# Kernel optimization log

Measured on AMD Instinct MI355X. Metric: run time of the kernel, lower is better.

## Reference

```python
import jax, jax.numpy as jnp
import numpy as np

B, T, E, H, P = 512, 512, 64, 128, 96


def setup_inputs() -> dict:
    key = jax.random.key(0)
    ks = jax.random.split(key, 12)
    s = 1.0 / np.sqrt(H)  # torch GRU/Linear uniform init scale
    u = lambda k, shape: jax.random.uniform(k, shape, jnp.float32, -s, s)
    return {
        "x": jax.random.normal(ks[0], (B, T, E), jnp.float32),
        "W_ih0": u(ks[1], (3 * H, E)),
        "W_hh0": u(ks[2], (3 * H, H)),
        "b_ih0": u(ks[3], (3 * H,)),
        "b_hh0": u(ks[4], (3 * H,)),
        "W_ih1": u(ks[5], (3 * H, H)),
        "W_hh1": u(ks[6], (3 * H, H)),
        "b_ih1": u(ks[7], (3 * H,)),
        "b_hh1": u(ks[8], (3 * H,)),
        "W_head": u(ks[9], (P, H)),
        "b_head": u(ks[10], (P,)),
    }


def _gru_layer(x, W_ih, W_hh, b_ih, b_hh):
    # x: [B, T, F]; PyTorch gate order: r, z, n
    Bn, Tn, _ = x.shape
    Hn = W_hh.shape[1]
    # precompute input-side gates for all timesteps: [B, T, 3H]
    xg = jnp.einsum('btf,gf->btg', x, W_ih) + b_ih

    def step(h, xg_t):
        hg = h @ W_hh.T + b_hh                      # [B, 3H]
        xr, xz, xn = jnp.split(xg_t, 3, axis=-1)
        hr, hz, hn = jnp.split(hg, 3, axis=-1)
        r = jax.nn.sigmoid(xr + hr)
        z = jax.nn.sigmoid(xz + hz)
        n = jnp.tanh(xn + r * hn)
        h_new = (1.0 - z) * n + z * h
        return h_new, h_new

    h0 = jnp.zeros((Bn, Hn), x.dtype)
    _, ys = jax.lax.scan(step, h0, jnp.swapaxes(xg, 0, 1))  # ys: [T, B, H]
    return jnp.swapaxes(ys, 0, 1)                            # [B, T, H]


def reference(x, W_ih0, W_hh0, b_ih0, b_hh0, W_ih1, W_hh1, b_ih1, b_hh1, W_head, b_head):
    h1 = _gru_layer(x, W_ih0, W_hh0, b_ih0, b_hh0)
    h2 = _gru_layer(h1, W_ih1, W_hh1, b_ih1, b_hh1)
    last = h2[:, -1, :]                   # [B, H]
    return last @ W_head.T + b_head       # [B, pred_len]
```

## Files before the change

### kernel.cpp

```cpp
#include <hip/hip_runtime.h>


#define B_SZ 512
#define T_SZ 512
#define E_SZ 64
#define H_SZ 128
#define P_SZ 96
#define NB   16
#define NGRP (B_SZ / NB)
#define LO_SCALE 2048.0f
#define LO_INV   (1.0f/2048.0f)
#define SC_SIG  (-1.44269504f)
#define SC_TANH (-2.88539008f)

typedef _Float16 half8 __attribute__((ext_vector_type(8)));
typedef float    f32x4 __attribute__((ext_vector_type(4)));

__device__ __forceinline__ float exp2_(float x) {
#if __has_builtin(__builtin_amdgcn_exp2f)
    return __builtin_amdgcn_exp2f(x);
#else
    return exp2f(x);
#endif
}
__device__ __forceinline__ float rcp_(float x) {
#if __has_builtin(__builtin_amdgcn_rcpf)
    return __builtin_amdgcn_rcpf(x);
#else
    return 1.0f / x;
#endif
}

__device__ __forceinline__ int swz256(int row, int byte) {
    return row * 256 + (byte ^ ((row & 7) << 4));
}

__device__ __forceinline__ void load_bfrag(const float* __restrict__ W, int ldk,
                                           int n0, int kt, int ln, float scale,
                                           half8* hi, half8* lo) {
    int n = n0 + (ln & 15);
    int k = kt * 32 + (ln >> 4) * 8;
    const float* p = W + (size_t)n * ldk + k;
    float4 a = *(const float4*)p;
    float4 b = *(const float4*)(p + 4);
    float v[8] = {a.x, a.y, a.z, a.w, b.x, b.y, b.z, b.w};
    half8 h, l;
    #pragma unroll
    for (int j = 0; j < 8; ++j) {
        float w = v[j] * scale;
        _Float16 hh = (_Float16)w;
        h[j] = hh;
        l[j] = (_Float16)((w - (float)hh) * LO_SCALE);
    }
    *hi = h;
    if (lo) *lo = l;
}

#define LOADX(Sx, tt)                                                              \
    if ((tt) < T_SZ) {                                                             \
        _Pragma("unroll") for (int kt = 0; kt < KFX; ++kt)                         \
            Sx[kt] = *(const half8*)(xlane + (size_t)(tt) * ROWB + kt * 64);       \
    }

#define GRU_STEP(Sx, tcur, tnext)                                                  \
    {                                                                              \
        const char* hb = hs[(tcur) & 1];                                           \
        half8 ah[4];                                                               \
        _Pragma("unroll") for (int kt = 0; kt < 4; ++kt)                           \
            ah[kt] = *(const half8*)(hb + swz256(colg, kt * 64 + rgrp * 16));      \
        f32x4 ax0 = {bs0, bs0, bs0, bs0};                                          \
        f32x4 ax1 = {bs1, bs1, bs1, bs1};                                          \
        f32x4 ax2 = {bi2s, bi2s, bi2s, bi2s};                                      \
        f32x4 ah2 = {bh2s, bh2s, bh2s, bh2s};                                      \
        f32x4 ah0 = {0.f, 0.f, 0.f, 0.f};                                          \
        f32x4 ah1 = ah0, al2 = ah0;                                                \
        _Pragma("unroll") for (int kt = 0; kt < KFX; ++kt) {                       \
            ax0 = __builtin_amdgcn_mfma_f32_16x16x32_f16(Sx[kt], bx[0][kt], ax0, 0, 0, 0); \
            ax1 = __builtin_amdgcn_mfma_f32_16x16x32_f16(Sx[kt], bx[1][kt], ax1, 0, 0, 0); \
            ax2 = __builtin_amdgcn_mfma_f32_16x16x32_f16(Sx[kt], bx[2][kt], ax2, 0, 0, 0); \
        }                                                                          \
        _Pragma("unroll") for (int kt = 0; kt < 4; ++kt) {                         \
            ah0 = __builtin_amdgcn_mfma_f32_16x16x32_f16(ah[kt], bhh[0][kt], ah0, 0, 0, 0); \
            ah1 = __builtin_amdgcn_mfma_f32_16x16x32_f16(ah[kt], bhh[1][kt], ah1, 0, 0, 0); \
            ah2 = __builtin_amdgcn_mfma_f32_16x16x32_f16(ah[kt], bhh[2][kt], ah2, 0, 0, 0); \
            al2 = __builtin_amdgcn_mfma_f32_16x16x32_f16(ah[kt], bhl2[kt],   al2, 0, 0, 0); \
        }                                                                          \
        LOADX(Sx, tnext)                                                           \
        float hn_[4];                                                              \
        _Pragma("unroll") for (int j = 0; j < 4; ++j) {                            \
            float e0 = exp2_(ax0[j] + ah0[j]);                                     \
            float rr = rcp_(1.f + e0);                                             \
            float e1 = exp2_(ax1[j] + ah1[j]);                                     \
            float zz = rcp_(1.f + e1);                                             \
            float hnv = ah2[j] + al2[j] * LO_INV;                                  \
            float v  = ax2[j] + rr * hnv;                                          \
            v = fminf(fmaxf(v, -60.f), 60.f);                                      \
            float e2 = exp2_(v);                                                   \
            float nn = (1.f - e2) * rcp_(1.f + e2);                                \
            hn_[j] = nn + zz * (hreg[j] - nn);                                     \
            hreg[j] = hn_[j];                                                      \
        }                                                                          \
        char* hw = hs[((tcur) + 1) & 1];                                           \
        _Pragma("unroll") for (int j = 0; j < 4; ++j) {                            \
            int bb = rgrp * 4 + j;                                                 \
            *(_Float16*)(hw + swz256(bb, cw * 2)) = (_Float16)hn_[j];              \
            if constexpr (OUT_ALL) {                                               \
                ((_Float16*)hout)[((size_t)(b0 + bb) * T_SZ + (tcur)) * H_SZ + cw] \
                    = (_Float16)hn_[j];                                            \
            } else {                                                               \
                if ((tcur) == T_SZ - 1)                                            \
                    ((float*)hout)[(size_t)(b0 + bb) * H_SZ + cw] = hn_[j];        \
            }                                                                      \
        }                                                                          \
           \
        asm volatile("s_waitcnt lgkmcnt(0)" ::: "memory");                         \
        __builtin_amdgcn_s_barrier();                                              \
        __builtin_amdgcn_sched_barrier(0);                                         \
    }

template<int K_IN, bool OUT_ALL, int ROLE>
__device__ __forceinline__ void gru_body(const _Float16* __restrict__ xin,
                                         const float* __restrict__ W_ih,
                                         const float* __restrict__ W_hh,
                                         const float* __restrict__ b_ih,
                                         const float* __restrict__ b_hh,
                                         void* __restrict__ hout,
                                         int* __restrict__ prog,
                                         int grp, char (*hs)[4096])
{
    constexpr int KFX  = K_IN / 32;
    constexpr int ROWB = K_IN * 2;

    const int tid  = threadIdx.x;
    const int ln   = tid & 63;
    const int wv   = tid >> 6;
    const int colg = ln & 15;
    const int rgrp = ln >> 4;
    const int b0   = grp * NB;
    const int cw   = wv * 16 + colg;

    half8 bx[3][KFX];
    half8 bhh[3][4];
    half8 bhl2[4];
    const float gsc[3] = {SC_SIG, SC_SIG, SC_TANH};
    #pragma unroll
    for (int g = 0; g < 3; ++g) {
        int n0 = g * 128 + wv * 16;
        #pragma unroll
        for (int kt = 0; kt < KFX; ++kt)
            load_bfrag(W_ih, K_IN, n0, kt, ln, gsc[g], &bx[g][kt], nullptr);
        #pragma unroll
        for (int kt = 0; kt < 4; ++kt)
            load_bfrag(W_hh, H_SZ, n0, kt, ln, gsc[g], &bhh[g][kt],
                       (g == 2) ? &bhl2[kt] : nullptr);
    }
    const float bs0  = SC_SIG  * (b_ih[cw] + b_hh[cw]);
    const float bs1  = SC_SIG  * (b_ih[128 + cw] + b_hh[128 + cw]);
    const float bi2s = SC_TANH * b_ih[256 + cw];
    const float bh2s = SC_TANH * b_hh[256 + cw];

    if (tid < 256) *(float4*)(hs[0] + tid * 16) = make_float4(0.f, 0.f, 0.f, 0.f);
    float hreg[4] = {0.f, 0.f, 0.f, 0.f};

    const char* xlane = (const char*)xin
        + (size_t)(b0 + colg) * T_SZ * ROWB
        + rgrp * 16;

    int avail = 0;
    if (ROLE == 1) {
        while (avail < 4) {
            avail = __hip_atomic_load(prog, __ATOMIC_ACQUIRE, __HIP_MEMORY_SCOPE_AGENT);
            if (avail < 4) __builtin_amdgcn_s_sleep(8);
        }
    }

    half8 Ax[KFX], Bx2[KFX];
    LOADX(Ax, 0)
    LOADX(Bx2, 1)
    __syncthreads();

    for (int t = 0; t < T_SZ; t += 2) {
        if (ROLE == 1 && avail < T_SZ) {
            const int need = (t + 4 < T_SZ) ? t + 4 : T_SZ;
            while (avail < need) {
                avail = __hip_atomic_load(prog, __ATOMIC_ACQUIRE, __HIP_MEMORY_SCOPE_AGENT);
                if (avail < need) __builtin_amdgcn_s_sleep(8);
            }
        }
        GRU_STEP(Ax,  t,     t + 2)
        GRU_STEP(Bx2, t + 1, t + 3)
        if (ROLE == 0 && (t & 7) == 6) {
            asm volatile("s_waitcnt vmcnt(0)" ::: "memory");
            __builtin_amdgcn_s_barrier();
            if (tid == 0)
                __hip_atomic_store(prog, t + 2, __ATOMIC_RELEASE, __HIP_MEMORY_SCOPE_AGENT);
        }
    }
}

__global__ __launch_bounds__(512)
void gru_fused(const _Float16* __restrict__ xh,
               _Float16* __restrict__ h1,
               float* __restrict__ h2,
               const float* __restrict__ W_ih0, const float* __restrict__ W_hh0,
               const float* __restrict__ b_ih0, const float* __restrict__ b_hh0,
               const float* __restrict__ W_ih1, const float* __restrict__ W_hh1,
               const float* __restrict__ b_ih1, const float* __restrict__ b_hh1,
               int* __restrict__ prog)
{
    __shared__ __align__(16) char hs[2][4096];
    const int role = blockIdx.x >> 5;
    const int grp  = blockIdx.x & 31;
    if (role == 0)
        gru_body<E_SZ, true, 0>(xh, W_ih0, W_hh0, b_ih0, b_hh0, h1, prog + grp, grp, hs);
    else
        gru_body<H_SZ, false, 1>(h1, W_ih1, W_hh1, b_ih1, b_hh1, h2, prog + grp, grp, hs);
}

__global__ __launch_bounds__(256)
void cvt_f32_f16(const float* __restrict__ in, _Float16* __restrict__ out, int n8)
{
    int i = blockIdx.x * 256 + threadIdx.x;
    if (i >= n8) return;
    const float4* p = (const float4*)in + (size_t)i * 2;
    float4 a = p[0];
    float4 b = p[1];
    half8 h;
    h[0] = (_Float16)a.x; h[1] = (_Float16)a.y; h[2] = (_Float16)a.z; h[3] = (_Float16)a.w;
    h[4] = (_Float16)b.x; h[5] = (_Float16)b.y; h[6] = (_Float16)b.z; h[7] = (_Float16)b.w;
    ((half8*)out)[i] = h;
}

__global__ __launch_bounds__(256)
void head_kernel(const float* __restrict__ h2,
                 const float* __restrict__ W,
                 const float* __restrict__ bias,
                 float* __restrict__ out)
{
    int idx = blockIdx.x * 256 + threadIdx.x;
    if (idx >= B_SZ * P_SZ) return;
    int b = idx / P_SZ;
    int p = idx % P_SZ;
    const float* hv = h2 + b * H_SZ;
    const float* wv = W + p * H_SZ;
    float a0 = 0.f, a1 = 0.f, a2 = 0.f, a3 = 0.f;
    #pragma unroll
    for (int i = 0; i < H_SZ; i += 4) {
        float4 h4 = *(const float4*)(hv + i);
        float4 w4 = *(const float4*)(wv + i);
        a0 += h4.x * w4.x;
        a1 += h4.y * w4.y;
        a2 += h4.z * w4.z;
        a3 += h4.w * w4.w;
    }
    out[idx] = (a0 + a1) + (a2 + a3) + bias[p];
}

extern "C" void kernel_launch(void* const* d_in, const int* in_sizes, int n_in,
                              void* d_out, int out_size, void* d_ws, size_t ws_size,
                              hipStream_t stream)
{
    const float* x      = (const float*)d_in[0];
    const float* W_ih0  = (const float*)d_in[1];
    const float* W_hh0  = (const float*)d_in[2];
    const float* b_ih0  = (const float*)d_in[3];
    const float* b_hh0  = (const float*)d_in[4];
    const float* W_ih1  = (const float*)d_in[5];
    const float* W_hh1  = (const float*)d_in[6];
    const float* b_ih1  = (const float*)d_in[7];
    const float* b_hh1  = (const float*)d_in[8];
    const float* W_head = (const float*)d_in[9];
    const float* b_head = (const float*)d_in[10];
    float* out = (float*)d_out;

    char* ws = (char*)d_ws;
    _Float16* h1  = (_Float16*)ws;
    _Float16* xh  = (_Float16*)(ws + (64u << 20));
    float*    h2  = (float*)   (ws + (96u << 20));
    int*      prg = (int*)     (ws + (96u << 20) + (256u << 10));

    hipMemsetAsync(prg, 0, NGRP * sizeof(int), stream);
    cvt_f32_f16<<<(B_SZ * T_SZ * E_SZ / 8 + 255) / 256, 256, 0, stream>>>(x, xh, B_SZ * T_SZ * E_SZ / 8);
    gru_fused<<<2 * NGRP, 512, 0, stream>>>(xh, h1, h2,
                                            W_ih0, W_hh0, b_ih0, b_hh0,
                                            W_ih1, W_hh1, b_ih1, b_hh1, prg);
    head_kernel<<<(B_SZ * P_SZ + 255) / 256, 256, 0, stream>>>(h2, W_head, b_head, out);
}
```

Measured before the change: 524.3 us.

## Fuse fp32 input conversion into GRU, precompute input projections one step ahead

Removes the separate fp32-to-fp16 conversion kernel; layer 0 now loads fp32 x directly and converts in registers. The input-side MFMA projections for step t+1 are computed during step t, taking them off the serial recurrence path. Layer-0 output h1 is stored time-major for more contiguous access by layer 1, and the progress flag is published inside the step with a shorter sleep when polling. This adds register pressure and doubles the bytes read for x per step in layer 0.

```diff
diff --git a/kernel.cpp b/kernel.cpp
--- a/kernel.cpp
+++ b/kernel.cpp
@@ -56,44 +56,66 @@
     if (lo) *lo = l;
 }
 
-#define LOADX(Sx, tt)                                                              \
+#define LOADX(XH, XF, tt)                                                          \
     if ((tt) < T_SZ) {                                                             \
-        _Pragma("unroll") for (int kt = 0; kt < KFX; ++kt)                         \
-            Sx[kt] = *(const half8*)(xlane + (size_t)(tt) * ROWB + kt * 64);       \
-    }
-
-#define GRU_STEP(Sx, tcur, tnext)                                                  \
+        if constexpr (XF16) {                                                      \
+            _Pragma("unroll") for (int kt = 0; kt < KFX; ++kt)                     \
+                XH[kt] = *(const half8*)(xlane + (size_t)(tt) * TSTRIDE + kt * 64);\
+        } else {                                                                   \
+            _Pragma("unroll") for (int kt = 0; kt < KFX; ++kt) {                   \
+                XF[kt][0] = *(const float4*)(xlane + (size_t)(tt) * TSTRIDE + kt * 128);      \
+                XF[kt][1] = *(const float4*)(xlane + (size_t)(tt) * TSTRIDE + kt * 128 + 16); \
+            }                                                                      \
+        }                                                                          \
+    }
+
+#define CVTX(axf, XH, XF)                                                          \
+    if constexpr (XF16) {                                                          \
+        _Pragma("unroll") for (int kt = 0; kt < KFX; ++kt) axf[kt] = XH[kt];       \
+    } else {                                                                       \
+        _Pragma("unroll") for (int kt = 0; kt < KFX; ++kt) {                       \
+            half8 a;                                                               \
+            a[0] = (_Float16)XF[kt][0].x; a[1] = (_Float16)XF[kt][0].y;            \
+            a[2] = (_Float16)XF[kt][0].z; a[3] = (_Float16)XF[kt][0].w;            \
+            a[4] = (_Float16)XF[kt][1].x; a[5] = (_Float16)XF[kt][1].y;            \
+            a[6] = (_Float16)XF[kt][1].z; a[7] = (_Float16)XF[kt][1].w;            \
+            axf[kt] = a;                                                           \
+        }                                                                          \
+    }
+
+#define GRU_STEP(XdH, XdF, XlH, XlF, PR, PZ, PNX, QR, QZ, QNX, tcur)               \
     {                                                                              \
         const char* hb = hs[(tcur) & 1];                                           \
         half8 ah[4];                                                               \
         _Pragma("unroll") for (int kt = 0; kt < 4; ++kt)                           \
             ah[kt] = *(const half8*)(hb + swz256(colg, kt * 64 + rgrp * 16));      \
-        f32x4 ax0 = {bs0, bs0, bs0, bs0};                                          \
-        f32x4 ax1 = {bs1, bs1, bs1, bs1};                                          \
-        f32x4 ax2 = {bi2s, bi2s, bi2s, bi2s};                                      \
-        f32x4 ah2 = {bh2s, bh2s, bh2s, bh2s};                                      \
-        f32x4 ah0 = {0.f, 0.f, 0.f, 0.f};                                          \
-        f32x4 ah1 = ah0, al2 = ah0;                                                \
-        _Pragma("unroll") for (int kt = 0; kt < KFX; ++kt) {                       \
-            ax0 = __builtin_amdgcn_mfma_f32_16x16x32_f16(Sx[kt], bx[0][kt], ax0, 0, 0, 0); \
-            ax1 = __builtin_amdgcn_mfma_f32_16x16x32_f16(Sx[kt], bx[1][kt], ax1, 0, 0, 0); \
-            ax2 = __builtin_amdgcn_mfma_f32_16x16x32_f16(Sx[kt], bx[2][kt], ax2, 0, 0, 0); \
-        }                                                                          \
+        LOADX(XdH, XdF, (tcur) + 2)                                                \
+        QR  = (f32x4){bs0, bs0, bs0, bs0};                                         \
+        QZ  = (f32x4){bs1, bs1, bs1, bs1};                                         \
+        QNX = (f32x4){bi2s, bi2s, bi2s, bi2s};                                     \
+        {                                                                          \
+            half8 axf[KFX];                                                        \
+            CVTX(axf, XlH, XlF)                                                    \
+            _Pragma("unroll") for (int kt = 0; kt < KFX; ++kt) {                   \
+                QR  = __builtin_amdgcn_mfma_f32_16x16x32_f16(axf[kt], bxr[kt], QR,  0, 0, 0); \
+                QZ  = __builtin_amdgcn_mfma_f32_16x16x32_f16(axf[kt], bxz[kt], QZ,  0, 0, 0); \
+                QNX = __builtin_amdgcn_mfma_f32_16x16x32_f16(axf[kt], bxn[kt], QNX, 0, 0, 0); \
+            }                                                                      \
+        }                                                                          \
+        f32x4 cNH = {bh2s, bh2s, bh2s, bh2s};                                      \
+        f32x4 cNL = {0.f, 0.f, 0.f, 0.f};                                          \
         _Pragma("unroll") for (int kt = 0; kt < 4; ++kt) {                         \
-            ah0 = __builtin_amdgcn_mfma_f32_16x16x32_f16(ah[kt], bhh[0][kt], ah0, 0, 0, 0); \
-            ah1 = __builtin_amdgcn_mfma_f32_16x16x32_f16(ah[kt], bhh[1][kt], ah1, 0, 0, 0); \
-            ah2 = __builtin_amdgcn_mfma_f32_16x16x32_f16(ah[kt], bhh[2][kt], ah2, 0, 0, 0); \
-            al2 = __builtin_amdgcn_mfma_f32_16x16x32_f16(ah[kt], bhl2[kt],   al2, 0, 0, 0); \
-        }                                                                          \
-        LOADX(Sx, tnext)                                                           \
+            PR  = __builtin_amdgcn_mfma_f32_16x16x32_f16(ah[kt], bhr[kt], PR,  0, 0, 0); \
+            PZ  = __builtin_amdgcn_mfma_f32_16x16x32_f16(ah[kt], bhz[kt], PZ,  0, 0, 0); \
+            cNH = __builtin_amdgcn_mfma_f32_16x16x32_f16(ah[kt], bhn[kt], cNH, 0, 0, 0); \
+            cNL = __builtin_amdgcn_mfma_f32_16x16x32_f16(ah[kt], bhl[kt], cNL, 0, 0, 0); \
+        }                                                                          \
         float hn_[4];                                                              \
         _Pragma("unroll") for (int j = 0; j < 4; ++j) {                            \
-            float e0 = exp2_(ax0[j] + ah0[j]);                                     \
-            float rr = rcp_(1.f + e0);                                             \
-            float e1 = exp2_(ax1[j] + ah1[j]);                                     \
-            float zz = rcp_(1.f + e1);                                             \
-            float hnv = ah2[j] + al2[j] * LO_INV;                                  \
-            float v  = ax2[j] + rr * hnv;                                          \
+            float rr = rcp_(1.f + exp2_(PR[j]));                                   \
+            float zz = rcp_(1.f + exp2_(PZ[j]));                                   \
+            float hnv = cNH[j] + cNL[j] * LO_INV;                                  \
+            float v = PNX[j] + rr * hnv;                                           \
             v = fminf(fmaxf(v, -60.f), 60.f);                                      \
             float e2 = exp2_(v);                                                   \
             float nn = (1.f - e2) * rcp_(1.f + e2);                                \
@@ -105,21 +127,28 @@
             int bb = rgrp * 4 + j;                                                 \
             *(_Float16*)(hw + swz256(bb, cw * 2)) = (_Float16)hn_[j];              \
             if constexpr (OUT_ALL) {                                               \
-                ((_Float16*)hout)[((size_t)(b0 + bb) * T_SZ + (tcur)) * H_SZ + cw] \
+                ((_Float16*)hout)[((size_t)(tcur) * B_SZ + (b0 + bb)) * H_SZ + cw] \
                     = (_Float16)hn_[j];                                            \
             } else {                                                               \
                 if ((tcur) == T_SZ - 1)                                            \
                     ((float*)hout)[(size_t)(b0 + bb) * H_SZ + cw] = hn_[j];        \
             }                                                                      \
         }                                                                          \
-           \
-        asm volatile("s_waitcnt lgkmcnt(0)" ::: "memory");                         \
-        __builtin_amdgcn_s_barrier();                                              \
+        if (ROLE == 0 && (((tcur) & 7) == 7)) {                                    \
+            asm volatile("s_waitcnt vmcnt(0) lgkmcnt(0)" ::: "memory");            \
+            __builtin_amdgcn_s_barrier();                                          \
+            if (tid == 0)                                                          \
+                __hip_atomic_store(prog, (tcur) + 1, __ATOMIC_RELEASE,             \
+                                   __HIP_MEMORY_SCOPE_AGENT);                      \
+        } else {                                                                   \
+            asm volatile("s_waitcnt lgkmcnt(0)" ::: "memory");                     \
+            __builtin_amdgcn_s_barrier();                                          \
+        }                                                                          \
         __builtin_amdgcn_sched_barrier(0);                                         \
     }
 
-template<int K_IN, bool OUT_ALL, int ROLE>
-__device__ __forceinline__ void gru_body(const _Float16* __restrict__ xin,
+template<int K_IN, bool XF16, bool OUT_ALL, int ROLE, size_t TSTRIDE_>
+__device__ __forceinline__ void gru_body(const void* __restrict__ xin,
                                          const float* __restrict__ W_ih,
                                          const float* __restrict__ W_hh,
                                          const float* __restrict__ b_ih,
@@ -128,8 +157,8 @@
                                          int* __restrict__ prog,
                                          int grp, char (*hs)[4096])
 {
-    constexpr int KFX  = K_IN / 32;
-    constexpr int ROWB = K_IN * 2;
+    constexpr int    KFX     = K_IN / 32;
+    constexpr size_t TSTRIDE = TSTRIDE_;
 
     const int tid  = threadIdx.x;
     const int ln   = tid & 63;
@@ -139,20 +168,25 @@
     const int b0   = grp * NB;
     const int cw   = wv * 16 + colg;
 
-    half8 bx[3][KFX];
-    half8 bhh[3][4];
-    half8 bhl2[4];
-    const float gsc[3] = {SC_SIG, SC_SIG, SC_TANH};
-    #pragma unroll
-    for (int g = 0; g < 3; ++g) {
-        int n0 = g * 128 + wv * 16;
-        #pragma unroll
-        for (int kt = 0; kt < KFX; ++kt)
-            load_bfrag(W_ih, K_IN, n0, kt, ln, gsc[g], &bx[g][kt], nullptr);
-        #pragma unroll
-        for (int kt = 0; kt < 4; ++kt)
-            load_bfrag(W_hh, H_SZ, n0, kt, ln, gsc[g], &bhh[g][kt],
-                       (g == 2) ? &bhl2[kt] : nullptr);
+    half8 bxr[KFX], bxz[KFX], bxn[KFX];
+    half8 bhr[4], bhz[4], bhn[4], bhl[4];
+    {
+        int n0;
+        n0 = 0 * 128 + wv * 16;
+        #pragma unroll
+        for (int kt = 0; kt < KFX; ++kt) load_bfrag(W_ih, K_IN, n0, kt, ln, SC_SIG, &bxr[kt], nullptr);
+        #pragma unroll
+        for (int kt = 0; kt < 4; ++kt)   load_bfrag(W_hh, H_SZ, n0, kt, ln, SC_SIG, &bhr[kt], nullptr);
+        n0 = 1 * 128 + wv * 16;
+        #pragma unroll
+        for (int kt = 0; kt < KFX; ++kt) load_bfrag(W_ih, K_IN, n0, kt, ln, SC_SIG, &bxz[kt], nullptr);
+        #pragma unroll
+        for (int kt = 0; kt < 4; ++kt)   load_bfrag(W_hh, H_SZ, n0, kt, ln, SC_SIG, &bhz[kt], nullptr);
+        n0 = 2 * 128 + wv * 16;
+        #pragma unroll
+        for (int kt = 0; kt < KFX; ++kt) load_bfrag(W_ih, K_IN, n0, kt, ln, SC_TANH, &bxn[kt], nullptr);
+        #pragma unroll
+        for (int kt = 0; kt < 4; ++kt)   load_bfrag(W_hh, H_SZ, n0, kt, ln, SC_TANH, &bhn[kt], &bhl[kt]);
     }
     const float bs0  = SC_SIG  * (b_ih[cw] + b_hh[cw]);
     const float bs1  = SC_SIG  * (b_ih[128 + cw] + b_hh[128 + cw]);
@@ -163,43 +197,54 @@
     float hreg[4] = {0.f, 0.f, 0.f, 0.f};
 
     const char* xlane = (const char*)xin
-        + (size_t)(b0 + colg) * T_SZ * ROWB
-        + rgrp * 16;
+        + (XF16 ? ((size_t)(b0 + colg) * H_SZ * 2 + rgrp * 16)
+                : ((size_t)(b0 + colg) * T_SZ * E_SZ * 4 + rgrp * 32));
 
     int avail = 0;
     if (ROLE == 1) {
         while (avail < 4) {
             avail = __hip_atomic_load(prog, __ATOMIC_ACQUIRE, __HIP_MEMORY_SCOPE_AGENT);
-            if (avail < 4) __builtin_amdgcn_s_sleep(8);
+            if (avail < 4) __builtin_amdgcn_s_sleep(1);
         }
     }
 
-    half8 Ax[KFX], Bx2[KFX];
-    LOADX(Ax, 0)
-    LOADX(Bx2, 1)
+    half8  Xa[KFX], Xb[KFX];
+    float4 Xaf[KFX][2], Xbf[KFX][2];
+    LOADX(Xa, Xaf, 0)
+    LOADX(Xb, Xbf, 1)
+
+    f32x4 P0R, P0Z, P0NX, P1R, P1Z, P1NX;
+    P0R  = (f32x4){bs0, bs0, bs0, bs0};
+    P0Z  = (f32x4){bs1, bs1, bs1, bs1};
+    P0NX = (f32x4){bi2s, bi2s, bi2s, bi2s};
+    {
+        half8 axf[KFX];
+        CVTX(axf, Xa, Xaf)
+        #pragma unroll
+        for (int kt = 0; kt < KFX; ++kt) {
+            P0R  = __builtin_amdgcn_mfma_f32_16x16x32_f16(axf[kt], bxr[kt], P0R,  0, 0, 0);
+            P0Z  = __builtin_amdgcn_mfma_f32_16x16x32_f16(axf[kt], bxz[kt], P0Z,  0, 0, 0);
+            P0NX = __builtin_amdgcn_mfma_f32_16x16x32_f16(axf[kt], bxn[kt], P0NX, 0, 0, 0);
+        }
+    }
     __syncthreads();
 
     for (int t = 0; t < T_SZ; t += 2) {
         if (ROLE == 1 && avail < T_SZ) {
-            const int need = (t + 4 < T_SZ) ? t + 4 : T_SZ;
+            int need = t + 4;
+            if (need > T_SZ) need = T_SZ;
             while (avail < need) {
                 avail = __hip_atomic_load(prog, __ATOMIC_ACQUIRE, __HIP_MEMORY_SCOPE_AGENT);
-                if (avail < need) __builtin_amdgcn_s_sleep(8);
+                if (avail < need) __builtin_amdgcn_s_sleep(1);
             }
         }
-        GRU_STEP(Ax,  t,     t + 2)
-        GRU_STEP(Bx2, t + 1, t + 3)
-        if (ROLE == 0 && (t & 7) == 6) {
-            asm volatile("s_waitcnt vmcnt(0)" ::: "memory");
-            __builtin_amdgcn_s_barrier();
-            if (tid == 0)
-                __hip_atomic_store(prog, t + 2, __ATOMIC_RELEASE, __HIP_MEMORY_SCOPE_AGENT);
-        }
+        GRU_STEP(Xa, Xaf, Xb, Xbf, P0R, P0Z, P0NX, P1R, P1Z, P1NX, t)
+        GRU_STEP(Xb, Xbf, Xa, Xaf, P1R, P1Z, P1NX, P0R, P0Z, P0NX, t + 1)
     }
 }
 
 __global__ __launch_bounds__(512)
-void gru_fused(const _Float16* __restrict__ xh,
+void gru_fused(const float* __restrict__ x,
                _Float16* __restrict__ h1,
                float* __restrict__ h2,
                const float* __restrict__ W_ih0, const float* __restrict__ W_hh0,
@@ -212,23 +257,11 @@
     const int role = blockIdx.x >> 5;
     const int grp  = blockIdx.x & 31;
     if (role == 0)
-        gru_body<E_SZ, true, 0>(xh, W_ih0, W_hh0, b_ih0, b_hh0, h1, prog + grp, grp, hs);
+        gru_body<E_SZ, false, true, 0, (size_t)E_SZ * 4>(
+            x, W_ih0, W_hh0, b_ih0, b_hh0, h1, prog + grp, grp, hs);
     else
-        gru_body<H_SZ, false, 1>(h1, W_ih1, W_hh1, b_ih1, b_hh1, h2, prog + grp, grp, hs);
-}
-
-__global__ __launch_bounds__(256)
-void cvt_f32_f16(const float* __restrict__ in, _Float16* __restrict__ out, int n8)
-{
-    int i = blockIdx.x * 256 + threadIdx.x;
-    if (i >= n8) return;
-    const float4* p = (const float4*)in + (size_t)i * 2;
-    float4 a = p[0];
-    float4 b = p[1];
-    half8 h;
-    h[0] = (_Float16)a.x; h[1] = (_Float16)a.y; h[2] = (_Float16)a.z; h[3] = (_Float16)a.w;
-    h[4] = (_Float16)b.x; h[5] = (_Float16)b.y; h[6] = (_Float16)b.z; h[7] = (_Float16)b.w;
-    ((half8*)out)[i] = h;
+        gru_body<H_SZ, true, false, 1, (size_t)B_SZ * H_SZ * 2>(
+            h1, W_ih1, W_hh1, b_ih1, b_hh1, h2, prog + grp, grp, hs);
 }
 
 __global__ __launch_bounds__(256)
@@ -275,13 +308,11 @@
 
     char* ws = (char*)d_ws;
     _Float16* h1  = (_Float16*)ws;
-    _Float16* xh  = (_Float16*)(ws + (64u << 20));
-    float*    h2  = (float*)   (ws + (96u << 20));
-    int*      prg = (int*)     (ws + (96u << 20) + (256u << 10));
+    float*    h2  = (float*)   (ws + (64u << 20));
+    int*      prg = (int*)     (ws + (64u << 20) + (256u << 10));
 
     hipMemsetAsync(prg, 0, NGRP * sizeof(int), stream);
-    cvt_f32_f16<<<(B_SZ * T_SZ * E_SZ / 8 + 255) / 256, 256, 0, stream>>>(x, xh, B_SZ * T_SZ * E_SZ / 8);
-    gru_fused<<<2 * NGRP, 512, 0, stream>>>(xh, h1, h2,
+    gru_fused<<<2 * NGRP, 512, 0, stream>>>(x, h1, h2,
                                             W_ih0, W_hh0, b_ih0, b_hh0,
                                             W_ih1, W_hh1, b_ih1, b_hh1, prg);
     head_kernel<<<(B_SZ * P_SZ + 255) / 256, 256, 0, stream>>>(h2, W_head, b_head, out);
```

New measurement: 726.2 us. 38.5% more time.
